# Performance work log

Hardware: AMD Instinct MI355X
Metric: run time of the kernel (lower is better)

The kernel has to match this reference:

```python
import jax, jax.numpy as jnp
import numpy as np

B, V, S, H = 16384, 16, 64, 512


def setup_inputs() -> dict:
    key = jax.random.key(0)
    kx, kw, kb, kws, kbs = jax.random.split(key, 5)
    x = jax.random.normal(kx, (B, V, S), dtype=jnp.float32)
    # per-variable linear layers: weight [V, S, H], bias [V, H]
    W = jax.random.normal(kw, (V, S, H), dtype=jnp.float32) * (1.0 / np.sqrt(S))
    b = jax.random.normal(kb, (V, H), dtype=jnp.float32) * 0.01
    # variable selection linear: hidden -> V
    W_sel = jax.random.normal(kws, (H, V), dtype=jnp.float32) * (1.0 / np.sqrt(H))
    b_sel = jax.random.normal(kbs, (V,), dtype=jnp.float32) * 0.01
    return {"x": x, "W": W, "b": b, "W_sel": W_sel, "b_sel": b_sel}


def reference(x, W, b, W_sel, b_sel):
    # per-variable linears: [B, V, H]
    transformed = jnp.einsum('bvs,vsh->bvh', x, W) + b  # grouped small GEMMs
    # torch stacks to [B, H, V]; mean over variable axis -> [B, H]
    flat = transformed.mean(axis=1)
    # softmax-gated selection weights [B, V] (dropout is identity in eval)
    weights = jax.nn.softmax(flat @ W_sel + b_sel, axis=-1)
    # weighted sum over variables -> [B, H]
    out = jnp.einsum('bvh,bv->bh', transformed, weights)
    return out
```

## Files before the change

### kernel.cpp

```cpp
#include <hip/hip_runtime.h>
#include <hip/hip_bf16.h>
#include <stdint.h>

#define B_ROWS 16384
#define VDIM   16
#define SDIM   64
#define HDIM   512
#define KDIM   1024
#define KP     1056

using bf16x8 = __attribute__((ext_vector_type(8))) __bf16;
using u16x8  = __attribute__((ext_vector_type(8))) unsigned short;
using f32x4  = __attribute__((ext_vector_type(4))) float;

__device__ __forceinline__ unsigned short f2bf(float f) {
  unsigned int u = __builtin_bit_cast(unsigned int, f);
  u = (u + 0x7FFFu + ((u >> 16) & 1u)) >> 16;
  return (unsigned short)u;
}

__device__ __forceinline__ void gl_lds16(const void* g, void* l) {
  __builtin_amdgcn_global_load_lds(
      (const __attribute__((address_space(1))) void*)(g),
      (__attribute__((address_space(3))) void*)(l),
      16, 0, 0);
}

__global__ __launch_bounds__(256) void k0_prep(
    const float* __restrict__ W, const float* __restrict__ bias,
    const float* __restrict__ Wsel, const float* __restrict__ bsel,
    unsigned short* __restrict__ Bt, unsigned short* __restrict__ WcombT,
    float* __restrict__ bcomb) {
  __shared__ float wsl[512 * 17];
  __shared__ float bm[HDIM];
  __shared__ float part[16][17];
  const int t = threadIdx.x;
  if (blockIdx.x < 2112) {
    int idx = blockIdx.x * 256 + t;
    int k = idx >> 9;
    int n = idx & 511;
    float val;
    if (k < KDIM)            val = W[(size_t)k * HDIM + n];
    else if (k < KDIM + 16)  val = bias[(size_t)(k - KDIM) * HDIM + n];
    else                     val = 0.f;
    Bt[(size_t)n * KP + k] = f2bf(val);
    return;
  }
  const int bid = blockIdx.x - 2112;
  if (bid < 256) {
    for (int i = t; i < 512 * 16; i += 256) {
      int h = i >> 4, v = i & 15;
      wsl[h * 17 + v] = Wsel[i];
    }
    __syncthreads();
    const int wave = t >> 6, lane = t & 63;
    const int k = bid * 4 + wave;
    const float* wr = W + (size_t)k * HDIM;
    float s[16];
    #pragma unroll
    for (int v = 0; v < 16; ++v) s[v] = 0.f;
    #pragma unroll
    for (int j = 0; j < 8; ++j) {
      const int h = lane + 64 * j;
      const float a = wr[h];
      const float* wl = &wsl[h * 17];
      #pragma unroll
      for (int v = 0; v < 16; ++v) s[v] = fmaf(a, wl[v], s[v]);
    }
    #pragma unroll
    for (int off = 32; off > 0; off >>= 1) {
      #pragma unroll
      for (int v = 0; v < 16; ++v) s[v] += __shfl_xor(s[v], off, 64);
    }
    float mine = 0.f;
    #pragma unroll
    for (int v = 0; v < 16; ++v) mine = (lane == v) ? s[v] : mine;
    if (lane < 16) WcombT[lane * KDIM + k] = f2bf(mine * (1.f / 16.f));
  } else {
    for (int h = t; h < HDIM; h += 256) {
      float s = 0.f;
      #pragma unroll
      for (int v = 0; v < VDIM; ++v) s += bias[v * HDIM + h];
      bm[h] = s * (1.f / 16.f);
    }
    __syncthreads();
    int v = t & 15, sl = t >> 4;
    float s = 0.f;
    for (int h = sl * 32; h < sl * 32 + 32; ++h) s = fmaf(bm[h], Wsel[h * VDIM + v], s);
    part[sl][v] = s;
    __syncthreads();
    if (t < 16) {
      float s2 = bsel[t];
      #pragma unroll
      for (int i = 0; i < 16; ++i) s2 += part[i][t];
      bcomb[t] = s2;
    }
  }
}

__global__ __launch_bounds__(256) void k1a_logits(
    const float* __restrict__ x, const unsigned short* __restrict__ WcombT,
    float* __restrict__ part) {
  const int gw = blockIdx.x * 4 + (threadIdx.x >> 6);
  const int lane = threadIdx.x & 63;
  const int rt = gw >> 2, seg = gw & 3;
  const int m = lane & 15, quad = lane >> 4;
  const float* xr = x + (size_t)(rt * 16 + m) * KDIM + seg * 256 + quad * 8;
  const unsigned short* br = WcombT + m * KDIM + seg * 256 + quad * 8;
  f32x4 acc = {0.f, 0.f, 0.f, 0.f};
  #pragma unroll
  for (int kt = 0; kt < 8; ++kt) {
    float4 a0 = *(const float4*)(xr);
    float4 a1 = *(const float4*)(xr + 4);
    xr += 32;
    u16x8 u;
    u[0] = f2bf(a0.x); u[1] = f2bf(a0.y); u[2] = f2bf(a0.z); u[3] = f2bf(a0.w);
    u[4] = f2bf(a1.x); u[5] = f2bf(a1.y); u[6] = f2bf(a1.z); u[7] = f2bf(a1.w);
    bf16x8 af = __builtin_bit_cast(bf16x8, u);
    bf16x8 bfv = *(const bf16x8*)(br);
    br += 32;
    acc = __builtin_amdgcn_mfma_f32_16x16x32_bf16(af, bfv, acc, 0, 0, 0);
  }
  float* pr = part + (size_t)(rt * 16 + quad * 4) * 64 + seg * 16 + m;
  #pragma unroll
  for (int r = 0; r < 4; ++r) pr[(size_t)r * 64] = acc[r];
}

__global__ __launch_bounds__(256) void k1b0_softmax(
    const float* __restrict__ part, const float* __restrict__ bcomb,
    float* __restrict__ weights) {
  const int row = blockIdx.x * 256 + threadIdx.x;
  const float* p = part + (size_t)row * 64;
  float l[16];
  float mx = -1e30f;
  #pragma unroll
  for (int v = 0; v < 16; ++v) {
    l[v] = bcomb[v] + p[v] + p[16 + v] + p[32 + v] + p[48 + v];
    mx = fmaxf(mx, l[v]);
  }
  float s = 0.f;
  #pragma unroll
  for (int v = 0; v < 16; ++v) { l[v] = __expf(l[v] - mx); s += l[v]; }
  const float inv = 1.f / s;
  float4* wout = (float4*)(weights + (size_t)row * 16);
  #pragma unroll
  for (int q = 0; q < 4; ++q) {
    float4 f;
    f.x = l[4 * q + 0] * inv; f.y = l[4 * q + 1] * inv;
    f.z = l[4 * q + 2] * inv; f.w = l[4 * q + 3] * inv;
    wout[q] = f;
  }
}

__global__ __launch_bounds__(256, 4) void k2f_gemm(
    const float* __restrict__ x, const float* __restrict__ wts,
    const unsigned short* __restrict__ Bt, float* __restrict__ C) {
  __shared__ unsigned short As[64 * 40];
  __shared__ unsigned short Bs[128 * 32];

  const int t = threadIdx.x;
  const int wave = t >> 6, lane = t & 63;
  const int tm = blockIdx.x >> 2, tn = blockIdx.x & 3;
  const int mlane = lane & 15, quad = lane >> 4;
  const int wr = wave >> 1, wc = wave & 1;

  const int arow = t >> 2;
  const int kq = (t & 3) * 8;
  const int grow = tm * 64 + arow;
  const float* xrow = x + (size_t)grow * KDIM + kq;
  const float* wrow = wts + (size_t)grow * 16;
  unsigned short* asw = &As[arow * 40 + kq];

  const int c0 = wave * 2;
  const int nrow = lane >> 2;
  const int ksw = ((lane & 3) ^ (nrow & 3)) * 8;
  const unsigned short* bg0 = Bt + (size_t)(tn * 128 + (c0 + 0) * 16 + nrow) * KP + ksw;
  const unsigned short* bg1 = Bt + (size_t)(tn * 128 + (c0 + 1) * 16 + nrow) * KP + ksw;
  unsigned short* bsd0 = &Bs[(c0 + 0) * 16 * 32];
  unsigned short* bsd1 = &Bs[(c0 + 1) * 16 * 32];

  const unsigned short* ap[2];
  #pragma unroll
  for (int i = 0; i < 2; ++i)
    ap[i] = &As[(wr * 32 + i * 16 + mlane) * 40 + quad * 8];
  const unsigned short* bp[4];
  #pragma unroll
  for (int j = 0; j < 4; ++j) {
    const int nl = wc * 64 + j * 16 + mlane;
    bp[j] = &Bs[nl * 32 + ((quad ^ (mlane & 3)) * 8)];
  }

  f32x4 acc[2][4];
  const f32x4 z = {0.f, 0.f, 0.f, 0.f};
  #pragma unroll
  for (int i = 0; i < 2; ++i)
    #pragma unroll
    for (int j = 0; j < 4; ++j) acc[i][j] = z;

  for (int kt = 0; kt < 33; ++kt) {
    gl_lds16(bg0, bsd0);
    gl_lds16(bg1, bsd1);
    bg0 += 32; bg1 += 32;
    float vals[8];
    if (kt < 32) {
      const float4 a0 = *(const float4*)(xrow);
      const float4 a1 = *(const float4*)(xrow + 4);
      xrow += 32;
      const float w = wrow[kt >> 1];
      vals[0] = w * a0.x; vals[1] = w * a0.y; vals[2] = w * a0.z; vals[3] = w * a0.w;
      vals[4] = w * a1.x; vals[5] = w * a1.y; vals[6] = w * a1.z; vals[7] = w * a1.w;
    } else {
      if (kq < 16) {
        const float4 w0 = *(const float4*)(wrow + kq);
        const float4 w1 = *(const float4*)(wrow + kq + 4);
        vals[0] = w0.x; vals[1] = w0.y; vals[2] = w0.z; vals[3] = w0.w;
        vals[4] = w1.x; vals[5] = w1.y; vals[6] = w1.z; vals[7] = w1.w;
      } else {
        #pragma unroll
        for (int j = 0; j < 8; ++j) vals[j] = 0.f;
      }
    }
    u16x8 u;
    #pragma unroll
    for (int j = 0; j < 8; ++j) u[j] = f2bf(vals[j]);
    *(u16x8*)asw = u;

    __syncthreads();
    bf16x8 af[2], bfv[4];
    #pragma unroll
    for (int i = 0; i < 2; ++i) af[i]  = *(const bf16x8*)ap[i];
    #pragma unroll
    for (int j = 0; j < 4; ++j) bfv[j] = *(const bf16x8*)bp[j];
    #pragma unroll
    for (int i = 0; i < 2; ++i)
      #pragma unroll
      for (int j = 0; j < 4; ++j)
        acc[i][j] = __builtin_amdgcn_mfma_f32_16x16x32_bf16(af[i], bfv[j], acc[i][j], 0, 0, 0);
    __syncthreads();
  }

  const size_t rowb = (size_t)(tm * 64 + wr * 32);
  const int colb = tn * 128 + wc * 64;
  #pragma unroll
  for (int i = 0; i < 2; ++i)
    #pragma unroll
    for (int j = 0; j < 4; ++j)
      #pragma unroll
      for (int r = 0; r < 4; ++r) {
        const size_t row = rowb + i * 16 + quad * 4 + r;
        const int col = colb + j * 16 + mlane;
        C[row * HDIM + col] = acc[i][j][r];
      }
}

extern "C" void kernel_launch(void* const* d_in, const int* in_sizes, int n_in,
                              void* d_out, int out_size, void* d_ws, size_t ws_size,
                              hipStream_t stream) {
  const float* x    = (const float*)d_in[0];
  const float* W    = (const float*)d_in[1];
  const float* bias = (const float*)d_in[2];
  const float* Wsel = (const float*)d_in[3];
  const float* bsel = (const float*)d_in[4];
  float* out = (float*)d_out;

  char* ws = (char*)d_ws;
  unsigned short* Bt     = (unsigned short*)(ws);
  unsigned short* WcombT = (unsigned short*)(ws + 1081344);
  float*          bcomb  = (float*)(ws + 1114112);
  float*          part   = (float*)(ws + 1114368);
  float*          wts    = (float*)(ws + 5308672);

  k0_prep<<<2369, 256, 0, stream>>>(W, bias, Wsel, bsel, Bt, WcombT, bcomb);
  k1a_logits<<<1024, 256, 0, stream>>>(x, WcombT, part);
  k1b0_softmax<<<64, 256, 0, stream>>>(part, bcomb, wts);
  k2f_gemm<<<1024, 256, 0, stream>>>(x, wts, Bt, out);
}
```

Before: 182.9 us.

## Stage full A row-block in LDS once and stream B fragments from global

The GEMM kernel now uses 512-thread blocks that each own 64 rows and all 512 columns. Every block scales and converts its whole 64x1056 A slab to bf16 into dynamic LDS once (about 136 KB), so x is read from DRAM exactly once instead of four times. B fragments are then loaded directly from global/L2 into registers each k-step, with no per-step barriers. The costs are only 256 blocks, high LDS usage per block, no overlap between the staging phase and the MFMA work, and B reads that depend on L2 hits and have exposed latency.

New measurement: 163.5 us. 1.12x faster.

```diff
diff --git a/kernel.cpp b/kernel.cpp
--- a/kernel.cpp
+++ b/kernel.cpp
@@ -8,6 +8,8 @@
 #define HDIM   512
 #define KDIM   1024
 #define KP     1056
+#define ASTR   1064
+#define K2_LDS (64 * ASTR * 2)
 
 using bf16x8 = __attribute__((ext_vector_type(8))) __bf16;
 using u16x8  = __attribute__((ext_vector_type(8))) unsigned short;
@@ -17,13 +19,6 @@
   unsigned int u = __builtin_bit_cast(unsigned int, f);
   u = (u + 0x7FFFu + ((u >> 16) & 1u)) >> 16;
   return (unsigned short)u;
-}
-
-__device__ __forceinline__ void gl_lds16(const void* g, void* l) {
-  __builtin_amdgcn_global_load_lds(
-      (const __attribute__((address_space(1))) void*)(g),
-      (__attribute__((address_space(3))) void*)(l),
-      16, 0, 0);
 }
 
 __global__ __launch_bounds__(256) void k0_prep(
@@ -152,102 +147,87 @@
   }
 }
 
-__global__ __launch_bounds__(256, 4) void k2f_gemm(
+__global__ __launch_bounds__(512, 2) void k2f_gemm(
     const float* __restrict__ x, const float* __restrict__ wts,
     const unsigned short* __restrict__ Bt, float* __restrict__ C) {
-  __shared__ unsigned short As[64 * 40];
-  __shared__ unsigned short Bs[128 * 32];
+  extern __shared__ unsigned short As[];
 
   const int t = threadIdx.x;
+  const int rowb = blockIdx.x * 64;
+
+  {
+    const int srow = t >> 3;
+    const int sc = (t & 7) * 4;
+    const float* xr = x + (size_t)(rowb + srow) * KDIM + sc;
+    const float* wr = wts + (size_t)(rowb + srow) * 16;
+    float wv[16];
+    #pragma unroll
+    for (int q = 0; q < 4; ++q) {
+      float4 f = ((const float4*)wr)[q];
+      wv[4 * q + 0] = f.x; wv[4 * q + 1] = f.y; wv[4 * q + 2] = f.z; wv[4 * q + 3] = f.w;
+    }
+    unsigned short* aw = As + srow * ASTR + sc;
+    #pragma unroll 4
+    for (int i = 0; i < 32; ++i) {
+      const float4 a = *(const float4*)(xr + i * 32);
+      const float w = wv[i >> 1];
+      unsigned short o[4];
+      o[0] = f2bf(w * a.x); o[1] = f2bf(w * a.y);
+      o[2] = f2bf(w * a.z); o[3] = f2bf(w * a.w);
+      *(uint2*)(aw + i * 32) = *(const uint2*)o;
+    }
+    if ((t & 7) < 4) {
+      const int j8 = (t & 7) * 8;
+      unsigned short o[8];
+      #pragma unroll
+      for (int jj = 0; jj < 8; ++jj)
+        o[jj] = (j8 + jj < 16) ? f2bf(wv[j8 + jj]) : (unsigned short)0;
+      *(u16x8*)(As + srow * ASTR + KDIM + j8) = *(const u16x8*)o;
+    }
+  }
+  __syncthreads();
+
   const int wave = t >> 6, lane = t & 63;
-  const int tm = blockIdx.x >> 2, tn = blockIdx.x & 3;
   const int mlane = lane & 15, quad = lane >> 4;
-  const int wr = wave >> 1, wc = wave & 1;
-
-  const int arow = t >> 2;
-  const int kq = (t & 3) * 8;
-  const int grow = tm * 64 + arow;
-  const float* xrow = x + (size_t)grow * KDIM + kq;
-  const float* wrow = wts + (size_t)grow * 16;
-  unsigned short* asw = &As[arow * 40 + kq];
-
-  const int c0 = wave * 2;
-  const int nrow = lane >> 2;
-  const int ksw = ((lane & 3) ^ (nrow & 3)) * 8;
-  const unsigned short* bg0 = Bt + (size_t)(tn * 128 + (c0 + 0) * 16 + nrow) * KP + ksw;
-  const unsigned short* bg1 = Bt + (size_t)(tn * 128 + (c0 + 1) * 16 + nrow) * KP + ksw;
-  unsigned short* bsd0 = &Bs[(c0 + 0) * 16 * 32];
-  unsigned short* bsd1 = &Bs[(c0 + 1) * 16 * 32];
-
-  const unsigned short* ap[2];
-  #pragma unroll
-  for (int i = 0; i < 2; ++i)
-    ap[i] = &As[(wr * 32 + i * 16 + mlane) * 40 + quad * 8];
+  const int colb = wave * 64;
+
   const unsigned short* bp[4];
   #pragma unroll
-  for (int j = 0; j < 4; ++j) {
-    const int nl = wc * 64 + j * 16 + mlane;
-    bp[j] = &Bs[nl * 32 + ((quad ^ (mlane & 3)) * 8)];
-  }
-
-  f32x4 acc[2][4];
+  for (int j = 0; j < 4; ++j)
+    bp[j] = Bt + (size_t)(colb + j * 16 + mlane) * KP + quad * 8;
+  const unsigned short* ap[4];
+  #pragma unroll
+  for (int i = 0; i < 4; ++i)
+    ap[i] = As + (i * 16 + mlane) * ASTR + quad * 8;
+
+  f32x4 acc[4][4];
   const f32x4 z = {0.f, 0.f, 0.f, 0.f};
   #pragma unroll
-  for (int i = 0; i < 2; ++i)
+  for (int i = 0; i < 4; ++i)
     #pragma unroll
     for (int j = 0; j < 4; ++j) acc[i][j] = z;
 
+  #pragma unroll 1
   for (int kt = 0; kt < 33; ++kt) {
-    gl_lds16(bg0, bsd0);
-    gl_lds16(bg1, bsd1);
-    bg0 += 32; bg1 += 32;
-    float vals[8];
-    if (kt < 32) {
-      const float4 a0 = *(const float4*)(xrow);
-      const float4 a1 = *(const float4*)(xrow + 4);
-      xrow += 32;
-      const float w = wrow[kt >> 1];
-      vals[0] = w * a0.x; vals[1] = w * a0.y; vals[2] = w * a0.z; vals[3] = w * a0.w;
-      vals[4] = w * a1.x; vals[5] = w * a1.y; vals[6] = w * a1.z; vals[7] = w * a1.w;
-    } else {
-      if (kq < 16) {
-        const float4 w0 = *(const float4*)(wrow + kq);
-        const float4 w1 = *(const float4*)(wrow + kq + 4);
-        vals[0] = w0.x; vals[1] = w0.y; vals[2] = w0.z; vals[3] = w0.w;
-        vals[4] = w1.x; vals[5] = w1.y; vals[6] = w1.z; vals[7] = w1.w;
-      } else {
-        #pragma unroll
-        for (int j = 0; j < 8; ++j) vals[j] = 0.f;
-      }
-    }
-    u16x8 u;
-    #pragma unroll
-    for (int j = 0; j < 8; ++j) u[j] = f2bf(vals[j]);
-    *(u16x8*)asw = u;
-
-    __syncthreads();
-    bf16x8 af[2], bfv[4];
-    #pragma unroll
-    for (int i = 0; i < 2; ++i) af[i]  = *(const bf16x8*)ap[i];
-    #pragma unroll
-    for (int j = 0; j < 4; ++j) bfv[j] = *(const bf16x8*)bp[j];
-    #pragma unroll
-    for (int i = 0; i < 2; ++i)
+    bf16x8 bv[4], av[4];
+    #pragma unroll
+    for (int j = 0; j < 4; ++j) { bv[j] = *(const bf16x8*)bp[j]; bp[j] += 32; }
+    #pragma unroll
+    for (int i = 0; i < 4; ++i) { av[i] = *(const bf16x8*)ap[i]; ap[i] += 32; }
+    #pragma unroll
+    for (int i = 0; i < 4; ++i)
       #pragma unroll
       for (int j = 0; j < 4; ++j)
-        acc[i][j] = __builtin_amdgcn_mfma_f32_16x16x32_bf16(af[i], bfv[j], acc[i][j], 0, 0, 0);
-    __syncthreads();
-  }
-
-  const size_t rowb = (size_t)(tm * 64 + wr * 32);
-  const int colb = tn * 128 + wc * 64;
-  #pragma unroll
-  for (int i = 0; i < 2; ++i)
+        acc[i][j] = __builtin_amdgcn_mfma_f32_16x16x32_bf16(av[i], bv[j], acc[i][j], 0, 0, 0);
+  }
+
+  #pragma unroll
+  for (int i = 0; i < 4; ++i)
     #pragma unroll
     for (int j = 0; j < 4; ++j)
       #pragma unroll
       for (int r = 0; r < 4; ++r) {
-        const size_t row = rowb + i * 16 + quad * 4 + r;
+        const size_t row = (size_t)rowb + i * 16 + quad * 4 + r;
         const int col = colb + j * 16 + mlane;
         C[row * HDIM + col] = acc[i][j][r];
       }
@@ -270,8 +250,15 @@
   float*          part   = (float*)(ws + 1114368);
   float*          wts    = (float*)(ws + 5308672);
 
+  static int lds_set = 0;
+  if (!lds_set) {
+    hipFuncSetAttribute((const void*)k2f_gemm,
+                        hipFuncAttributeMaxDynamicSharedMemorySize, K2_LDS);
+    lds_set = 1;
+  }
+
   k0_prep<<<2369, 256, 0, stream>>>(W, bias, Wsel, bsel, Bt, WcombT, bcomb);
   k1a_logits<<<1024, 256, 0, stream>>>(x, WcombT, part);
   k1b0_softmax<<<64, 256, 0, stream>>>(part, bcomb, wts);
-  k2f_gemm<<<1024, 256, 0, stream>>>(x, wts, Bt, out);
-}
+  k2f_gemm<<<256, 512, K2_LDS, stream>>>(x, wts, Bt, out);
+}
```
